# Kernel tuning notes

Hardware: AMD Instinct MI355X
Metric: run time of the kernel (lower is better)

Reference implementation:

```python
import jax, jax.numpy as jnp
import numpy as np

K = 15                # top-k codes per token
COMMITMENT_COST = 0.25
N, D, Q = 16384, 256, 8192  # tokens, embed_dim, quant_dim (codebook size)


def setup_inputs() -> dict:
    key = jax.random.key(0)
    k1, k2 = jax.random.split(key)
    z_e = jax.random.normal(k1, (N, D), dtype=jnp.float32)
    # codebook initialized uniform(-1/Q, 1/Q) as in the torch module
    embedding = jax.random.uniform(k2, (Q, D), dtype=jnp.float32,
                                   minval=-1.0 / Q, maxval=1.0 / Q)
    return {"z_e": z_e, "embedding": embedding}


def reference(z_e, embedding):
    # squared L2 distances: [N, Q]
    dist = (jnp.sum(z_e ** 2, axis=1, keepdims=True)
            - 2.0 * (z_e @ embedding.T)
            + jnp.sum(embedding ** 2, axis=1)[None, :])
    # top-k nearest codes (torch.topk(-dist))
    _, top_k_indices = jax.lax.top_k(-dist, K)           # [N, K] int32
    z_q_k = embedding[top_k_indices]                      # [N, K, D] gather
    # k-hot scatter: [N, Q]
    rows = jnp.arange(z_e.shape[0])[:, None]              # [N, 1]
    k_hot = jnp.zeros((z_e.shape[0], embedding.shape[0]), dtype=z_e.dtype)
    k_hot = k_hot.at[rows, top_k_indices].set(1.0)
    z_q = jnp.sum(z_q_k, axis=1)                          # [N, D]
    vq_loss = jnp.mean((z_q - jax.lax.stop_gradient(z_e)) ** 2)
    commitment_loss = jnp.mean((z_e - jax.lax.stop_gradient(z_q)) ** 2)
    total_vq_loss = vq_loss + COMMITMENT_COST * commitment_loss
    # straight-through estimator
    z_q_ste = z_e + jax.lax.stop_gradient(z_q - z_e)
    return (z_q_ste, total_vq_loss, k_hot)
```

## Files before the change

kernel.cpp:

```cpp
#include <hip/hip_runtime.h>


#pragma clang fp contract(off)

#define DIM   256
#define KSEL  15
#define CAP   160
#define NTC   64
#define KR    24

typedef short  s16x8 __attribute__((ext_vector_type(8)));
typedef float  f32x4 __attribute__((ext_vector_type(4)));

__device__ inline unsigned short f2bf(float f) {
  unsigned u = __builtin_bit_cast(unsigned, f);
  unsigned r = (u + 0x7FFFu + ((u >> 16) & 1u)) >> 16;
  return (unsigned short)r;
}

__global__ __launch_bounds__(256)
void prep(const float* __restrict__ emb, unsigned short* __restrict__ ebf,
          float* __restrict__ Enp, int Q) {
  const int gid = blockIdx.x * 256 + threadIdx.x;
  {
    const int i = gid * 8;
    float4 a = *(const float4*)(emb + i);
    float4 b = *(const float4*)(emb + i + 4);
    ushort4 o0; o0.x = f2bf(a.x); o0.y = f2bf(a.y); o0.z = f2bf(a.z); o0.w = f2bf(a.w);
    ushort4 o1; o1.x = f2bf(b.x); o1.y = f2bf(b.y); o1.z = f2bf(b.z); o1.w = f2bf(b.w);
    *(ushort4*)(ebf + i) = o0;
    *(ushort4*)(ebf + i + 4) = o1;
  }
  if (gid < Q) {
    const float* ep = emb + (size_t)gid * DIM;
    float Eh[2];
    for (int h = 0; h < 2; ++h) {
      const int base = 128 * h;
      float r[8];
#pragma unroll
      for (int q2 = 0; q2 < 8; ++q2) { float v = ep[base + q2]; r[q2] = v * v; }
      for (int i = 8; i < 128; i += 8)
#pragma unroll
        for (int q2 = 0; q2 < 8; ++q2) { float v = ep[base + i + q2]; float sq = v * v; r[q2] = r[q2] + sq; }
      Eh[h] = ((r[0] + r[1]) + (r[2] + r[3])) + ((r[4] + r[5]) + (r[6] + r[7]));
    }
    Enp[gid] = Eh[0] + Eh[1];
  }
}

__global__ __launch_bounds__(512, 2)
void vq_capture(const float* __restrict__ z, const unsigned short* __restrict__ ebf,
                int* __restrict__ cntg, unsigned short* __restrict__ candg,
                int N, int Q) {
  __shared__ union {
    unsigned short zbf[NTC][264];
    struct {
      unsigned short candL[NTC][CAP + 2];
      float          scL[NTC][CAP + 1];
    } c;
  } U;
  __shared__ int   cntL[NTC];
  __shared__ float tauL[NTC];
  __shared__ float red[512];

  const int tid  = threadIdx.x;
  const int lane = tid & 63;
  const int wv   = tid >> 6;
  const int t0   = blockIdx.x * NTC;

  {
    const int rt = tid >> 3, rq = tid & 7;
    const float* zp = z + (size_t)(t0 + rt) * DIM;
    float s = 0.f;
#pragma unroll
    for (int m = 0; m < 8; ++m) {
      float4 v = *(const float4*)(zp + 4 * rq + 32 * m);
      s = __builtin_fmaf(v.x, v.x, s);
      s = __builtin_fmaf(v.y, v.y, s);
      s = __builtin_fmaf(v.z, v.z, s);
      s = __builtin_fmaf(v.w, v.w, s);
      ushort4 o; o.x = f2bf(v.x); o.y = f2bf(v.y); o.z = f2bf(v.z); o.w = f2bf(v.w);
      *(ushort4*)&U.zbf[rt][4 * rq + 32 * m] = o;
    }
    red[tid] = s;
  }
  if (tid < NTC) cntL[tid] = 0;
  __syncthreads();

  if (tid < NTC) {
    float s = 0.f;
    for (int j = 0; j < 8; ++j) s += red[tid * 8 + j];
    const float a = 1.0f / (float)Q;
    tauL[tid] = 2.45f * a * 0.57735027f * sqrtf(s) - 1e-6f;
  }

  s16x8 afrag[4][8];
  {
    const int arow = lane & 15;
    const int kq   = (lane >> 4) * 8;
#pragma unroll
    for (int tt = 0; tt < 4; ++tt) {
#pragma unroll
      for (int ks = 0; ks < 8; ++ks)
        afrag[tt][ks] = *(const s16x8*)&U.zbf[tt * 16 + arow][ks * 32 + kq];
    }
  }
  __syncthreads();

  {
    const int ncw  = Q / 8;
    const int c0w  = wv * ncw;
    const int col  = lane & 15;
    const int kq8  = (lane >> 4) * 8;
    const int rbase = (lane >> 4) * 4;
    const unsigned short* bbase = ebf + ((size_t)(c0w + col) * DIM + kq8);

    uint4 buf0[8], buf1[8];
#pragma unroll
    for (int ks = 0; ks < 8; ++ks) buf0[ks] = *(const uint4*)(bbase + ks * 32);

    for (int it = 0; it < 64; it += 2) {
      {
        const unsigned short* bp = bbase + (size_t)(it + 1) * 16 * DIM;
#pragma unroll
        for (int ks = 0; ks < 8; ++ks) buf1[ks] = *(const uint4*)(bp + ks * 32);
      }
      {
        f32x4 acc0 = {0.f, 0.f, 0.f, 0.f};
        f32x4 acc1 = {0.f, 0.f, 0.f, 0.f};
        f32x4 acc2 = {0.f, 0.f, 0.f, 0.f};
        f32x4 acc3 = {0.f, 0.f, 0.f, 0.f};
#pragma unroll
        for (int ks = 0; ks < 8; ++ks) {
          s16x8 bfv = __builtin_bit_cast(s16x8, buf0[ks]);
          acc0 = __builtin_amdgcn_mfma_f32_16x16x32_bf16(afrag[0][ks], bfv, acc0, 0, 0, 0);
          acc1 = __builtin_amdgcn_mfma_f32_16x16x32_bf16(afrag[1][ks], bfv, acc1, 0, 0, 0);
          acc2 = __builtin_amdgcn_mfma_f32_16x16x32_bf16(afrag[2][ks], bfv, acc2, 0, 0, 0);
          acc3 = __builtin_amdgcn_mfma_f32_16x16x32_bf16(afrag[3][ks], bfv, acc3, 0, 0, 0);
        }
        const int code = c0w + it * 16 + col;
#pragma unroll
        for (int r = 0; r < 4; ++r) {
          const int tk0 = rbase + r;
          if (acc0[r] > tauL[tk0]) {
            int s = atomicAdd(&cntL[tk0], 1);
            if (s < CAP) { U.c.candL[tk0][s] = (unsigned short)code; U.c.scL[tk0][s] = acc0[r]; }
          }
          const int tk1 = 16 + rbase + r;
          if (acc1[r] > tauL[tk1]) {
            int s = atomicAdd(&cntL[tk1], 1);
            if (s < CAP) { U.c.candL[tk1][s] = (unsigned short)code; U.c.scL[tk1][s] = acc1[r]; }
          }
          const int tk2 = 32 + rbase + r;
          if (acc2[r] > tauL[tk2]) {
            int s = atomicAdd(&cntL[tk2], 1);
            if (s < CAP) { U.c.candL[tk2][s] = (unsigned short)code; U.c.scL[tk2][s] = acc2[r]; }
          }
          const int tk3 = 48 + rbase + r;
          if (acc3[r] > tauL[tk3]) {
            int s = atomicAdd(&cntL[tk3], 1);
            if (s < CAP) { U.c.candL[tk3][s] = (unsigned short)code; U.c.scL[tk3][s] = acc3[r]; }
          }
        }
      }
      if (it + 2 < 64) {
        const unsigned short* bp = bbase + (size_t)(it + 2) * 16 * DIM;
#pragma unroll
        for (int ks = 0; ks < 8; ++ks) buf0[ks] = *(const uint4*)(bp + ks * 32);
      }
      {
        f32x4 acc0 = {0.f, 0.f, 0.f, 0.f};
        f32x4 acc1 = {0.f, 0.f, 0.f, 0.f};
        f32x4 acc2 = {0.f, 0.f, 0.f, 0.f};
        f32x4 acc3 = {0.f, 0.f, 0.f, 0.f};
#pragma unroll
        for (int ks = 0; ks < 8; ++ks) {
          s16x8 bfv = __builtin_bit_cast(s16x8, buf1[ks]);
          acc0 = __builtin_amdgcn_mfma_f32_16x16x32_bf16(afrag[0][ks], bfv, acc0, 0, 0, 0);
          acc1 = __builtin_amdgcn_mfma_f32_16x16x32_bf16(afrag[1][ks], bfv, acc1, 0, 0, 0);
          acc2 = __builtin_amdgcn_mfma_f32_16x16x32_bf16(afrag[2][ks], bfv, acc2, 0, 0, 0);
          acc3 = __builtin_amdgcn_mfma_f32_16x16x32_bf16(afrag[3][ks], bfv, acc3, 0, 0, 0);
        }
        const int code = c0w + (it + 1) * 16 + col;
#pragma unroll
        for (int r = 0; r < 4; ++r) {
          const int tk0 = rbase + r;
          if (acc0[r] > tauL[tk0]) {
            int s = atomicAdd(&cntL[tk0], 1);
            if (s < CAP) { U.c.candL[tk0][s] = (unsigned short)code; U.c.scL[tk0][s] = acc0[r]; }
          }
          const int tk1 = 16 + rbase + r;
          if (acc1[r] > tauL[tk1]) {
            int s = atomicAdd(&cntL[tk1], 1);
            if (s < CAP) { U.c.candL[tk1][s] = (unsigned short)code; U.c.scL[tk1][s] = acc1[r]; }
          }
          const int tk2 = 32 + rbase + r;
          if (acc2[r] > tauL[tk2]) {
            int s = atomicAdd(&cntL[tk2], 1);
            if (s < CAP) { U.c.candL[tk2][s] = (unsigned short)code; U.c.scL[tk2][s] = acc2[r]; }
          }
          const int tk3 = 48 + rbase + r;
          if (acc3[r] > tauL[tk3]) {
            int s = atomicAdd(&cntL[tk3], 1);
            if (s < CAP) { U.c.candL[tk3][s] = (unsigned short)code; U.c.scL[tk3][s] = acc3[r]; }
          }
        }
      }
    }
  }
  __syncthreads();

  if ((tid & 7) == 0) {
    const int t = tid >> 3;
    const int m = min(cntL[t], CAP);
    const int keep = min(m, KR);
    for (int k = 0; k < keep; ++k) {
      float bv = -3.4e38f; int bj = 0;
      for (int j = 0; j < m; ++j) {
        float v = U.c.scL[t][j];
        if (v > bv) { bv = v; bj = j; }
      }
      U.c.scL[t][bj] = -3.5e38f;
      candg[(size_t)(t0 + t) * KR + k] = U.c.candL[t][bj];
    }
    cntg[t0 + t] = keep;
  }
}

__global__ __launch_bounds__(256, 4)
void vq_out(const float* __restrict__ z, const float* __restrict__ emb,
            const float* __restrict__ Enp, const int* __restrict__ cntg,
            const unsigned short* __restrict__ candg, float* __restrict__ out,
            int N, int Q) {
  __shared__ __align__(16) float zld[4][DIM + 4];
  __shared__ float red[256];

  const int tid  = threadIdx.x;
  const int lane = tid & 63;
  const int wv   = tid >> 6;
  const int gw   = blockIdx.x * 4 + wv;
  float* khot = out + (size_t)N * DIM + 1;

  float lpacc = 0.f;

  for (int ti = 0; ti < 4; ++ti) {
    const int t = gw * 4 + ti;

    {
      const float4 v = *(const float4*)(z + (size_t)t * DIM + 4 * lane);
      *(float4*)&zld[wv][4 * lane] = v;
    }
    const int mb = min(cntg[t], KR);
    const int c_mine = (lane < mb) ? (int)candg[(size_t)t * KR + lane] : 0;

    asm volatile("s_waitcnt lgkmcnt(0)" ::: "memory");
    __builtin_amdgcn_sched_barrier(0);

    float Arow;
    {
      float Aval = 0.f;
      if (lane == 0) {
        const float* zl = &zld[wv][0];
        float Ah[2];
        for (int h = 0; h < 2; ++h) {
          const int base = 128 * h;
          float r[8];
#pragma unroll
          for (int q2 = 0; q2 < 8; ++q2) { float v = zl[base + q2]; r[q2] = v * v; }
          for (int i = 8; i < 128; i += 8)
#pragma unroll
            for (int q2 = 0; q2 < 8; ++q2) { float v = zl[base + i + q2]; float sq = v * v; r[q2] = r[q2] + sq; }
          Ah[h] = ((r[0] + r[1]) + (r[2] + r[3])) + ((r[4] + r[5]) + (r[6] + r[7]));
        }
        Aval = Ah[0] + Ah[1];
      }
      Arow = __shfl(Aval, 0);
    }

    float scv = 3.4e38f;
    if (lane < mb) {
      const float* el = emb + (size_t)c_mine * DIM;
      const float* zl = &zld[wv][0];
      float bch = 0.f;
      for (int i = 0; i < 256; i += 8) {
        float4 ea = *(const float4*)(el + i);
        float4 eb = *(const float4*)(el + i + 4);
        float4 za = *(const float4*)(zl + i);
        float4 zb = *(const float4*)(zl + i + 4);
        bch = __builtin_fmaf(za.x, ea.x, bch);
        bch = __builtin_fmaf(za.y, ea.y, bch);
        bch = __builtin_fmaf(za.z, ea.z, bch);
        bch = __builtin_fmaf(za.w, ea.w, bch);
        bch = __builtin_fmaf(zb.x, eb.x, bch);
        bch = __builtin_fmaf(zb.y, eb.y, bch);
        bch = __builtin_fmaf(zb.z, eb.z, bch);
        bch = __builtin_fmaf(zb.w, eb.w, bch);
      }
      scv = (Arow - 2.0f * bch) + Enp[c_mine];
    }

    int mywin = 0;
    {
      unsigned okey = __builtin_bit_cast(unsigned, scv);
      okey = (okey & 0x80000000u) ? ~okey : (okey | 0x80000000u);
      unsigned long long key = (lane < mb)
          ? (((unsigned long long)okey << 32) | (unsigned)c_mine)
          : 0xFFFFFFFFFFFFFFFFull;
      for (int k = 0; k < KSEL; ++k) {
        unsigned long long m = key;
#pragma unroll
        for (int d = 1; d < 64; d <<= 1) {
          unsigned long long o = __shfl_xor(m, d);
          m = (o < m) ? o : m;
        }
        int wcode = ((unsigned)(m >> 32) == 0xFFFFFFFFu) ? 0 : (int)(unsigned)(m & 0xFFFFFFFFull);
        if (lane == k) mywin = wcode;
        if (key == m) key = 0xFFFFFFFFFFFFFFFFull;
      }
    }

    if (lane < KSEL) khot[(size_t)t * Q + mywin] = 1.0f;

    {
      float4 zq4 = make_float4(0.f, 0.f, 0.f, 0.f);
      for (int k = 0; k < KSEL; ++k) {
        const int c = __shfl(mywin, k);
        const float4 e4 = *(const float4*)(emb + (size_t)c * DIM + 4 * lane);
        zq4.x = zq4.x + e4.x; zq4.y = zq4.y + e4.y;
        zq4.z = zq4.z + e4.z; zq4.w = zq4.w + e4.w;
      }
      const float4 zv = *(const float4*)&zld[wv][4 * lane];
      float d0 = zq4.x - zv.x, d1 = zq4.y - zv.y, d2 = zq4.z - zv.z, d3 = zq4.w - zv.w;
      float4 o; o.x = zv.x + d0; o.y = zv.y + d1; o.z = zv.z + d2; o.w = zv.w + d3;
      *(float4*)(out + (size_t)t * DIM + 4 * lane) = o;
      lpacc = __builtin_fmaf(d0, d0, lpacc);
      lpacc = __builtin_fmaf(d1, d1, lpacc);
      lpacc = __builtin_fmaf(d2, d2, lpacc);
      lpacc = __builtin_fmaf(d3, d3, lpacc);
    }
  }

  red[tid] = lpacc;
  __syncthreads();
  for (int s = 128; s > 0; s >>= 1) {
    if (tid < s) red[tid] += red[tid + s];
    __syncthreads();
  }
  if (tid == 0) {
    const float scale = 1.25f / (float)((size_t)N * DIM);
    atomicAdd(out + (size_t)N * DIM, red[0] * scale);
  }
}

extern "C" void kernel_launch(void* const* d_in, const int* in_sizes, int n_in,
                              void* d_out, int out_size, void* d_ws, size_t ws_size,
                              hipStream_t stream) {
  const float* z   = (const float*)d_in[0];
  const float* emb = (const float*)d_in[1];
  float* out = (float*)d_out;
  const int N = in_sizes[0] / DIM;
  const int Q = in_sizes[1] / DIM;

  unsigned short* ebf = (unsigned short*)d_ws;
  char* p = (char*)d_ws + (size_t)Q * DIM * 2;
  float* Enp  = (float*)p;           p += (size_t)Q * 4;
  int*   cntg = (int*)p;             p += (size_t)N * 4;
  unsigned short* candg = (unsigned short*)p;

  hipMemsetAsync((char*)d_out + (size_t)N * DIM * sizeof(float), 0,
                 (1 + (size_t)N * Q) * sizeof(float), stream);
  prep<<<dim3((Q * DIM) / (8 * 256)), dim3(256), 0, stream>>>(emb, ebf, Enp, Q);
  vq_capture<<<dim3(N / NTC), dim3(512), 0, stream>>>(z, ebf, cntg, candg, N, Q);
  vq_out<<<dim3(N / 16), dim3(256), 0, stream>>>(z, emb, Enp, cntg, candg, out, N, Q);
}
```

Measured before the change: 888.3 us.

## Replace shared-memory atomic candidate capture with per-wave ballot appends

Threshold hits are no longer appended to per-token shared counters with atomicAdd. Each wave uses ballot/popcount ranks to append into its own per-wave candidate list, keeping the counts in registers. Each entry packs a bf16 score with the code index into one 32-bit word, so the final top-KR selection compares single unsigned integers across the 8 per-wave lists. This is meant to remove LDS atomic contention and divergence in the hot MFMA loop. In exchange it adds ballots on every accumulator row, caps each wave's list at 32 entries, and ranks candidates at bf16 score precision.

Measured after the change: 911.7 us. 2.6% more time.

```diff
diff --git a/kernel.cpp b/kernel.cpp
--- a/kernel.cpp
+++ b/kernel.cpp
@@ -5,7 +5,7 @@
 
 #define DIM   256
 #define KSEL  15
-#define CAP   160
+#define CAPW  32
 #define NTC   64
 #define KR    24
 
@@ -48,24 +48,45 @@
   }
 }
 
+#define GAPPEND(ACC, A) do {                                                  \
+    _Pragma("unroll")                                                         \
+    for (int r = 0; r < 4; ++r) {                                             \
+      const bool pr = (ACC)[r] > tauR[(A)][r];                                \
+      const unsigned long long bm = __ballot(pr);                             \
+      const unsigned gm = (unsigned)((bm >> (grp << 4)) & 0xFFFFull);         \
+      if (gm) {                                                               \
+        if (pr) {                                                             \
+          const int rank = __popc(gm & sublow);                               \
+          const int slot = cnt[(A)][r] + rank;                                \
+          if (slot < CAPW) {                                                  \
+            const int tk = (A) * 16 + (grp << 2) + r;                         \
+            U.candW[wv][tk][slot] =                                           \
+                (((unsigned)f2bf((ACC)[r])) << 16) | (unsigned)code;          \
+          }                                                                   \
+        }                                                                     \
+        cnt[(A)][r] += __popc(gm);                                            \
+      }                                                                       \
+    }                                                                         \
+  } while (0)
+
 __global__ __launch_bounds__(512, 2)
 void vq_capture(const float* __restrict__ z, const unsigned short* __restrict__ ebf,
                 int* __restrict__ cntg, unsigned short* __restrict__ candg,
                 int N, int Q) {
   __shared__ union {
     unsigned short zbf[NTC][264];
-    struct {
-      unsigned short candL[NTC][CAP + 2];
-      float          scL[NTC][CAP + 1];
-    } c;
+    unsigned int   candW[8][NTC][CAPW];
   } U;
-  __shared__ int   cntL[NTC];
+  __shared__ int   cntW[8][NTC];
   __shared__ float tauL[NTC];
   __shared__ float red[512];
 
   const int tid  = threadIdx.x;
   const int lane = tid & 63;
   const int wv   = tid >> 6;
+  const int grp  = lane >> 4;
+  const int sub  = lane & 15;
+  const unsigned sublow = (1u << sub) - 1u;
   const int t0   = blockIdx.x * NTC;
 
   {
@@ -84,7 +105,6 @@
     }
     red[tid] = s;
   }
-  if (tid < NTC) cntL[tid] = 0;
   __syncthreads();
 
   if (tid < NTC) {
@@ -96,8 +116,8 @@
 
   s16x8 afrag[4][8];
   {
-    const int arow = lane & 15;
-    const int kq   = (lane >> 4) * 8;
+    const int arow = sub;
+    const int kq   = grp * 8;
 #pragma unroll
     for (int tt = 0; tt < 4; ++tt) {
 #pragma unroll
@@ -106,13 +126,24 @@
     }
   }
   __syncthreads();
+
+  int cnt[4][4];
+#pragma unroll
+  for (int a = 0; a < 4; ++a)
+#pragma unroll
+    for (int r = 0; r < 4; ++r) cnt[a][r] = 0;
+
+  float tauR[4][4];
+#pragma unroll
+  for (int a = 0; a < 4; ++a)
+#pragma unroll
+    for (int r = 0; r < 4; ++r) tauR[a][r] = tauL[a * 16 + (grp << 2) + r];
 
   {
     const int ncw  = Q / 8;
     const int c0w  = wv * ncw;
-    const int col  = lane & 15;
-    const int kq8  = (lane >> 4) * 8;
-    const int rbase = (lane >> 4) * 4;
+    const int col  = sub;
+    const int kq8  = grp * 8;
     const unsigned short* bbase = ebf + ((size_t)(c0w + col) * DIM + kq8);
 
     uint4 buf0[8], buf1[8];
@@ -139,29 +170,10 @@
           acc3 = __builtin_amdgcn_mfma_f32_16x16x32_bf16(afrag[3][ks], bfv, acc3, 0, 0, 0);
         }
         const int code = c0w + it * 16 + col;
-#pragma unroll
-        for (int r = 0; r < 4; ++r) {
-          const int tk0 = rbase + r;
-          if (acc0[r] > tauL[tk0]) {
-            int s = atomicAdd(&cntL[tk0], 1);
-            if (s < CAP) { U.c.candL[tk0][s] = (unsigned short)code; U.c.scL[tk0][s] = acc0[r]; }
-          }
-          const int tk1 = 16 + rbase + r;
-          if (acc1[r] > tauL[tk1]) {
-            int s = atomicAdd(&cntL[tk1], 1);
-            if (s < CAP) { U.c.candL[tk1][s] = (unsigned short)code; U.c.scL[tk1][s] = acc1[r]; }
-          }
-          const int tk2 = 32 + rbase + r;
-          if (acc2[r] > tauL[tk2]) {
-            int s = atomicAdd(&cntL[tk2], 1);
-            if (s < CAP) { U.c.candL[tk2][s] = (unsigned short)code; U.c.scL[tk2][s] = acc2[r]; }
-          }
-          const int tk3 = 48 + rbase + r;
-          if (acc3[r] > tauL[tk3]) {
-            int s = atomicAdd(&cntL[tk3], 1);
-            if (s < CAP) { U.c.candL[tk3][s] = (unsigned short)code; U.c.scL[tk3][s] = acc3[r]; }
-          }
-        }
+        GAPPEND(acc0, 0);
+        GAPPEND(acc1, 1);
+        GAPPEND(acc2, 2);
+        GAPPEND(acc3, 3);
       }
       if (it + 2 < 64) {
         const unsigned short* bp = bbase + (size_t)(it + 2) * 16 * DIM;
@@ -182,46 +194,39 @@
           acc3 = __builtin_amdgcn_mfma_f32_16x16x32_bf16(afrag[3][ks], bfv, acc3, 0, 0, 0);
         }
         const int code = c0w + (it + 1) * 16 + col;
-#pragma unroll
-        for (int r = 0; r < 4; ++r) {
-          const int tk0 = rbase + r;
-          if (acc0[r] > tauL[tk0]) {
-            int s = atomicAdd(&cntL[tk0], 1);
-            if (s < CAP) { U.c.candL[tk0][s] = (unsigned short)code; U.c.scL[tk0][s] = acc0[r]; }
-          }
-          const int tk1 = 16 + rbase + r;
-          if (acc1[r] > tauL[tk1]) {
-            int s = atomicAdd(&cntL[tk1], 1);
-            if (s < CAP) { U.c.candL[tk1][s] = (unsigned short)code; U.c.scL[tk1][s] = acc1[r]; }
-          }
-          const int tk2 = 32 + rbase + r;
-          if (acc2[r] > tauL[tk2]) {
-            int s = atomicAdd(&cntL[tk2], 1);
-            if (s < CAP) { U.c.candL[tk2][s] = (unsigned short)code; U.c.scL[tk2][s] = acc2[r]; }
-          }
-          const int tk3 = 48 + rbase + r;
-          if (acc3[r] > tauL[tk3]) {
-            int s = atomicAdd(&cntL[tk3], 1);
-            if (s < CAP) { U.c.candL[tk3][s] = (unsigned short)code; U.c.scL[tk3][s] = acc3[r]; }
-          }
-        }
-      }
-    }
+        GAPPEND(acc0, 0);
+        GAPPEND(acc1, 1);
+        GAPPEND(acc2, 2);
+        GAPPEND(acc3, 3);
+      }
+    }
+  }
+
+  if (sub == 0) {
+#pragma unroll
+    for (int a = 0; a < 4; ++a)
+#pragma unroll
+      for (int r = 0; r < 4; ++r)
+        cntW[wv][a * 16 + (grp << 2) + r] = min(cnt[a][r], CAPW);
   }
   __syncthreads();
 
   if ((tid & 7) == 0) {
     const int t = tid >> 3;
-    const int m = min(cntL[t], CAP);
-    const int keep = min(m, KR);
-    for (int k = 0; k < keep; ++k) {
-      float bv = -3.4e38f; int bj = 0;
-      for (int j = 0; j < m; ++j) {
-        float v = U.c.scL[t][j];
-        if (v > bv) { bv = v; bj = j; }
-      }
-      U.c.scL[t][bj] = -3.5e38f;
-      candg[(size_t)(t0 + t) * KR + k] = U.c.candL[t][bj];
+    int keep = 0;
+    for (int k = 0; k < KR; ++k) {
+      unsigned best = 0; int bw = -1, bj = 0;
+      for (int w = 0; w < 8; ++w) {
+        const int mw = cntW[w][t];
+        for (int j = 0; j < mw; ++j) {
+          const unsigned v = U.candW[w][t][j];
+          if (v > best) { best = v; bw = w; bj = j; }
+        }
+      }
+      if (bw < 0) break;
+      U.candW[bw][t][bj] = 0;
+      candg[(size_t)(t0 + t) * KR + k] = (unsigned short)(best & 0xFFFFu);
+      keep++;
     }
     cntg[t0 + t] = keep;
   }
```
